# Performance work log

Measured on AMD Instinct MI355X. Metric: run time of the kernel, lower is better.

## Reference

```python
import jax, jax.numpy as jnp
import numpy as np
import math

B, N, D, H = 2, 2048, 512, 8
DH = D // H
HID = int(D * 16 / 3)  # 2730, SwiGLU hidden; chunks into 1365+1365
EPS = 1e-5


def _get_slopes(n):
    # n=8 is a power of two
    start = 2.0 ** (-2.0 ** (-(math.log2(n) - 3)))
    return np.array([start * (start ** i) for i in range(n)], dtype=np.float32)

_SLOPES = jnp.asarray(_get_slopes(H))  # [H]


def _ln(x, w, b):
    m = jnp.mean(x, axis=-1, keepdims=True)
    v = jnp.mean((x - m) ** 2, axis=-1, keepdims=True)
    return (x - m) * jax.lax.rsqrt(v + EPS) * w + b


def setup_inputs() -> dict:
    key = jax.random.key(0)
    ks = jax.random.split(key, 20)
    p = lambda k, s: jax.random.normal(k, s, jnp.float32) * 0.02
    return {
        "x": jax.random.normal(ks[0], (B, N, D), jnp.float32),
        "coords": jax.random.uniform(ks[1], (B, N, 2), jnp.float32) * 100.0,
        "q_w": p(ks[2], (D, D)), "q_b": jnp.zeros((D,), jnp.float32),
        "k_w": p(ks[3], (D, D)), "k_b": jnp.zeros((D,), jnp.float32),
        "v_w": p(ks[4], (D, D)), "v_b": jnp.zeros((D,), jnp.float32),
        "o_w": p(ks[5], (D, D)), "o_b": jnp.zeros((D,), jnp.float32),
        "gamma1": jnp.ones((D,), jnp.float32),
        "ln1_w": jnp.ones((D,), jnp.float32), "ln1_b": jnp.zeros((D,), jnp.float32),
        "fc1_w": p(ks[6], (HID, D)), "fc1_b": jnp.zeros((HID,), jnp.float32),
        "fc2_w": p(ks[7], (D, HID // 2)), "fc2_b": jnp.zeros((D,), jnp.float32),
        "gamma2": jnp.ones((D,), jnp.float32),
        "ln2_w": jnp.ones((D,), jnp.float32), "ln2_b": jnp.zeros((D,), jnp.float32),
    }


def reference(x, coords, q_w, q_b, k_w, k_b, v_w, v_b, o_w, o_b, gamma1,
              ln1_w, ln1_b, fc1_w, fc1_b, fc2_w, fc2_b, gamma2, ln2_w, ln2_b):
    # ---- residual1: distance-ALiBi attention (eval mode: x + gamma1*attn(norm(x)))
    xn = _ln(x, ln1_w, ln1_b)
    q = (xn @ q_w.T + q_b).reshape(B, N, H, DH).transpose(0, 2, 1, 3)  # [b,h,n,dh]
    k = (xn @ k_w.T + k_b).reshape(B, N, H, DH).transpose(0, 2, 1, 3)
    v = (xn @ v_w.T + v_b).reshape(B, N, H, DH).transpose(0, 2, 1, 3)
    # pairwise Euclidean distance of tile coords -> [b,n,n]
    diff = coords[:, :, None, :] - coords[:, None, :, :]
    dist = jnp.sqrt(jnp.sum(diff * diff, axis=-1))
    attn_bias = -_SLOPES[None, :, None, None] * dist[:, None, :, :]  # [b,h,n,n]
    scale = 1.0 / math.sqrt(DH)
    scores = jnp.einsum('bhqd,bhkd->bhqk', q, k) * scale + attn_bias
    attn = jax.nn.softmax(scores, axis=-1)
    ctx = jnp.einsum('bhqk,bhkd->bhqd', attn, v)
    ctx = ctx.transpose(0, 2, 1, 3).reshape(B, N, D)
    attn_out = ctx @ o_w.T + o_b
    x = x + gamma1 * attn_out
    # ---- residual2: SwiGLU-style MLP (eval mode: x + gamma2*mlp(norm(x)))
    xn2 = _ln(x, ln2_w, ln2_b)
    hpre = xn2 @ fc1_w.T + fc1_b  # [b,n,HID]
    h1, h2 = jnp.split(hpre, 2, axis=-1)
    mlp_out = (jax.nn.silu(h1) * h2) @ fc2_w.T + fc2_b
    return x + gamma2 * mlp_out
```

## Files before the change

kernel.cpp:

```cpp
#include <hip/hip_runtime.h>
#include <math.h>

#define Bdim  2
#define Nseq  2048
#define Dmod  512
#define Hn    8
#define DHd   64
#define HID   2730
#define HHALF 1365
#define HC    1408
#define NPACK 2816
#define ROWS  4096
#define NSPLIT 2
#define KT_PER (Nseq / 64 / NSPLIT)

typedef __bf16 bf16x8 __attribute__((ext_vector_type(8)));
typedef __bf16 bf16x4 __attribute__((ext_vector_type(4)));
typedef float  f32x4  __attribute__((ext_vector_type(4)));

__device__ __forceinline__ void glds16(const __bf16* g, __bf16* l) {
    __builtin_amdgcn_global_load_lds(
        (const __attribute__((address_space(1))) void*)g,
        (__attribute__((address_space(3))) void*)l, 16, 0, 0);
}

#define SEG0 (1536*512)
#define SEG1 (512*512)
#define SEG2 (NPACK*512)
#define SEG3 (512*HC)
__global__ __launch_bounds__(256) void convert_all(
    const float* __restrict__ q_w, const float* __restrict__ k_w,
    const float* __restrict__ v_w, const float* __restrict__ o_w,
    const float* __restrict__ fc1_w, const float* __restrict__ fc2_w,
    __bf16* __restrict__ wqkv, __bf16* __restrict__ wo,
    __bf16* __restrict__ wfc1p, __bf16* __restrict__ wfc2p)
{
    int idx = blockIdx.x * 256 + threadIdx.x;
    if (idx < SEG0) {
        int n = idx >> 9, k = idx & 511;
        float v = (n < 512) ? q_w[n * 512 + k]
                : (n < 1024) ? k_w[(n - 512) * 512 + k]
                : v_w[(n - 1024) * 512 + k];
        wqkv[idx] = (__bf16)v;
        return;
    }
    idx -= SEG0;
    if (idx < SEG1) { wo[idx] = (__bf16)o_w[idx]; return; }
    idx -= SEG1;
    if (idx < SEG2) {
        int n = idx >> 9, k = idx & 511;
        int j = n >> 5, u = n & 31;
        int base = j * 16 + (u & 15);
        float v = 0.0f;
        if (base < HHALF) {
            int hidx = base + ((u & 16) ? HHALF : 0);
            v = fc1_w[(size_t)hidx * 512 + k];
        }
        wfc1p[idx] = (__bf16)v;
        return;
    }
    idx -= SEG2;
    if (idx < SEG3) {
        int n = idx / HC, k = idx - n * HC;
        float v = (k < HHALF) ? fc2_w[(size_t)n * HHALF + k] : 0.0f;
        wfc2p[idx] = (__bf16)v;
    }
}

__global__ __launch_bounds__(256) void ln_kernel(
    const float* __restrict__ x, const float* __restrict__ w,
    const float* __restrict__ b, __bf16* __restrict__ out)
{
    const int row = blockIdx.x;
    const int tid = threadIdx.x;
    const float* xr = x + (size_t)row * Dmod;
    float2 v = *(const float2*)(xr + tid * 2);
    float s  = v.x + v.y;
    float sq = v.x * v.x + v.y * v.y;
#pragma unroll
    for (int m = 1; m < 64; m <<= 1) {
        s  += __shfl_xor(s, m, 64);
        sq += __shfl_xor(sq, m, 64);
    }
    __shared__ float ss[4], ssq[4];
    const int wv = tid >> 6;
    if ((tid & 63) == 0) { ss[wv] = s; ssq[wv] = sq; }
    __syncthreads();
    s  = ss[0] + ss[1] + ss[2] + ss[3];
    sq = ssq[0] + ssq[1] + ssq[2] + ssq[3];
    const float mean = s * (1.0f / Dmod);
    const float var  = sq * (1.0f / Dmod) - mean * mean;
    const float rstd = rsqrtf(var + 1e-5f);
    float2 wv2 = *(const float2*)(w + tid * 2);
    float2 bv2 = *(const float2*)(b + tid * 2);
    __bf16* orow = out + (size_t)row * Dmod + tid * 2;
    orow[0] = (__bf16)((v.x - mean) * rstd * wv2.x + bv2.x);
    orow[1] = (__bf16)((v.y - mean) * rstd * wv2.y + bv2.y);
}

__global__ __launch_bounds__(256) void gemm_res(
    const __bf16* __restrict__ A, int lda,
    const __bf16* __restrict__ Bw, int ldb,
    const float* __restrict__ bias, int K,
    float* __restrict__ out_f32, int ld_out,
    const float* __restrict__ res, const float* __restrict__ g)
{
    __shared__ __bf16 As[64][40];
    __shared__ __bf16 Bs[64][40];
    const int tid  = threadIdx.x;
    const int wave = tid >> 6, lane = tid & 63;
    const int t    = lane & 15, quad = lane >> 4;
    const int m0   = blockIdx.x * 64;
    const int n0   = blockIdx.y * 64;
    const int sr   = tid >> 2, sc = (tid & 3) * 8;

    f32x4 acc[4] = {};
    bf16x8 av = *(const bf16x8*)(A  + (size_t)(m0 + sr) * lda + sc);
    bf16x8 bv = *(const bf16x8*)(Bw + (size_t)(n0 + sr) * ldb + sc);

    for (int k0 = 0; k0 < K; k0 += 32) {
        __syncthreads();
        *(bf16x8*)(&As[sr][sc]) = av;
        *(bf16x8*)(&Bs[sr][sc]) = bv;
        __syncthreads();
        if (k0 + 32 < K) {
            av = *(const bf16x8*)(A  + (size_t)(m0 + sr) * lda + (k0 + 32 + sc));
            bv = *(const bf16x8*)(Bw + (size_t)(n0 + sr) * ldb + (k0 + 32 + sc));
        }
        bf16x8 a = *(const bf16x8*)(&As[wave * 16 + t][quad * 8]);
#pragma unroll
        for (int ct = 0; ct < 4; ++ct) {
            bf16x8 b = *(const bf16x8*)(&Bs[ct * 16 + t][quad * 8]);
            acc[ct] = __builtin_amdgcn_mfma_f32_16x16x32_bf16(a, b, acc[ct], 0, 0, 0);
        }
    }

    const int row_base = m0 + wave * 16 + quad * 4;
#pragma unroll
    for (int ct = 0; ct < 4; ++ct) {
        const int col = n0 + ct * 16 + t;
        const float bb = bias[col];
#pragma unroll
        for (int r = 0; r < 4; ++r) {
            const int row = row_base + r;
            out_f32[(size_t)row * ld_out + col] =
                res[(size_t)row * ld_out + col] + g[col] * (acc[ct][r] + bb);
        }
    }
}

__global__ __launch_bounds__(256) void qkv_gemm128(
    const __bf16* __restrict__ A, const __bf16* __restrict__ W,
    const float* __restrict__ qb_, const float* __restrict__ kb_,
    const float* __restrict__ vb_,
    __bf16* __restrict__ qk, __bf16* __restrict__ vtg)
{
    __shared__ __bf16 As[128 * 32];
    __shared__ __bf16 Bs[128 * 32];
    const int tid  = threadIdx.x;
    const int wave = tid >> 6, lane = tid & 63;
    const int t    = lane & 15, quad = lane >> 4;
    const int m0   = blockIdx.x * 128, n0 = blockIdx.y * 128;
    const int mr   = (wave & 1) * 64,  nr = (wave >> 1) * 64;
    const int ra0 = tid >> 2,          ca0 = (tid & 3) * 8;
    const int ra1 = (tid + 256) >> 2,  ca1 = (tid & 3) * 8;

    f32x4 acc[4][4] = {};

    for (int k0 = 0; k0 < Dmod; k0 += 32) {
        __syncthreads();
        glds16(A + (size_t)(m0 + ra0) * Dmod + k0 + ca0, As + tid * 8);
        glds16(A + (size_t)(m0 + ra1) * Dmod + k0 + ca1, As + (tid + 256) * 8);
        glds16(W + (size_t)(n0 + ra0) * Dmod + k0 + ca0, Bs + tid * 8);
        glds16(W + (size_t)(n0 + ra1) * Dmod + k0 + ca1, Bs + (tid + 256) * 8);
        __syncthreads();
        bf16x8 af[4], bfr[4];
#pragma unroll
        for (int mi = 0; mi < 4; ++mi)
            af[mi] = *(const bf16x8*)(As + (mr + mi * 16 + t) * 32 + quad * 8);
#pragma unroll
        for (int ni = 0; ni < 4; ++ni)
            bfr[ni] = *(const bf16x8*)(Bs + (nr + ni * 16 + t) * 32 + quad * 8);
#pragma unroll
        for (int mi = 0; mi < 4; ++mi)
#pragma unroll
            for (int ni = 0; ni < 4; ++ni)
                acc[mi][ni] = __builtin_amdgcn_mfma_f32_16x16x32_bf16(af[mi], bfr[ni], acc[mi][ni], 0, 0, 0);
    }

#pragma unroll
    for (int mi = 0; mi < 4; ++mi) {
        const int row_base = m0 + mr + mi * 16 + quad * 4;
#pragma unroll
        for (int ni = 0; ni < 4; ++ni) {
            const int col = n0 + nr + ni * 16 + t;
            const float bb = (col < 512) ? qb_[col]
                            : (col < 1024) ? kb_[col - 512] : vb_[col - 1024];
            if (col < 1024) {
#pragma unroll
                for (int r = 0; r < 4; ++r)
                    qk[(size_t)(row_base + r) * 1024 + col] = (__bf16)(acc[mi][ni][r] + bb);
            } else {
                const int f = col - 1024, hh = f >> 6, dh = f & 63;
                const int bI = row_base >> 11, n = row_base & 2047;
                bf16x4 pk;
#pragma unroll
                for (int r = 0; r < 4; ++r) pk[r] = (__bf16)(acc[mi][ni][r] + bb);
                *(bf16x4*)(vtg + ((size_t)((bI * 8 + hh) * 64 + dh)) * Nseq + n) = pk;
            }
        }
    }
}

__global__ __launch_bounds__(256) void fc1_gemm128(
    const __bf16* __restrict__ A, const __bf16* __restrict__ W,
    const float* __restrict__ fc1_b_, __bf16* __restrict__ out)
{
    __shared__ __bf16 As[128 * 32];
    __shared__ __bf16 Bs[128 * 32];
    const int tid  = threadIdx.x;
    const int wave = tid >> 6, lane = tid & 63;
    const int t    = lane & 15, quad = lane >> 4;
    const int m0   = blockIdx.x * 128, n0 = blockIdx.y * 128;
    const int mr   = (wave & 1) * 64,  nr = (wave >> 1) * 64;
    const int ra0 = tid >> 2,          ca0 = (tid & 3) * 8;
    const int ra1 = (tid + 256) >> 2,  ca1 = (tid & 3) * 8;

    f32x4 acc[4][4] = {};

    for (int k0 = 0; k0 < Dmod; k0 += 32) {
        __syncthreads();
        glds16(A + (size_t)(m0 + ra0) * Dmod + k0 + ca0, As + tid * 8);
        glds16(A + (size_t)(m0 + ra1) * Dmod + k0 + ca1, As + (tid + 256) * 8);
        glds16(W + (size_t)(n0 + ra0) * Dmod + k0 + ca0, Bs + tid * 8);
        glds16(W + (size_t)(n0 + ra1) * Dmod + k0 + ca1, Bs + (tid + 256) * 8);
        __syncthreads();
        bf16x8 af[4], bfr[4];
#pragma unroll
        for (int mi = 0; mi < 4; ++mi)
            af[mi] = *(const bf16x8*)(As + (mr + mi * 16 + t) * 32 + quad * 8);
#pragma unroll
        for (int ni = 0; ni < 4; ++ni)
            bfr[ni] = *(const bf16x8*)(Bs + (nr + ni * 16 + t) * 32 + quad * 8);
#pragma unroll
        for (int mi = 0; mi < 4; ++mi)
#pragma unroll
            for (int ni = 0; ni < 4; ++ni)
                acc[mi][ni] = __builtin_amdgcn_mfma_f32_16x16x32_bf16(af[mi], bfr[ni], acc[mi][ni], 0, 0, 0);
    }

#pragma unroll
    for (int mi = 0; mi < 4; ++mi) {
        const int row_base = m0 + mr + mi * 16 + quad * 4;
#pragma unroll
        for (int gI = 0; gI < 2; ++gI) {
            const int base = n0 + nr + gI * 32;
            const int hb = (base >> 5) * 16 + t;
            const bool valid = hb < HHALF;
            const float b1 = valid ? fc1_b_[hb] : 0.0f;
            const float b2 = valid ? fc1_b_[HHALF + hb] : 0.0f;
#pragma unroll
            for (int r = 0; r < 4; ++r) {
                float a = acc[mi][2 * gI][r] + b1;
                float c = acc[mi][2 * gI + 1][r] + b2;
                float sw = a / (1.0f + __expf(-a)) * c;
                out[(size_t)(row_base + r) * HC + hb] = (__bf16)sw;
            }
        }
    }
}

__global__ __launch_bounds__(256) void attn_kernel(
    const __bf16* __restrict__ qk, const __bf16* __restrict__ vt,
    const float* __restrict__ coords,
    float* __restrict__ op, float* __restrict__ lp)
{
    constexpr int LD = 72;
    __shared__ __bf16 Ks[64][LD];
    __shared__ __bf16 Vt[64][LD];
    __shared__ __bf16 Ps[64][LD];
    __shared__ float2 kco[64];

    const int qt = blockIdx.x, h = blockIdx.y;
    const int s = blockIdx.z >> 1, b = blockIdx.z & 1;
    const int bh = b * Hn + h;
    const int tid = threadIdx.x;
    const int wave = tid >> 6, lane = tid & 63;
    const int t = lane & 15, quad = lane >> 4;
    const float c1 = 0.125f * 1.44269504f;
    const float d1 = exp2f(-(float)(h + 1)) * 1.44269504f;
    const int kt0 = s * KT_PER, kt1 = kt0 + KT_PER;

    const int qrow = qt * 64 + wave * 16 + t;
    const size_t qbase = (size_t)(b * Nseq + qrow) * 1024 + h * DHd;
    bf16x8 bq0 = *(const bf16x8*)(qk + qbase + quad * 8);
    bf16x8 bq1 = *(const bf16x8*)(qk + qbase + 32 + quad * 8);
    float2 qc = *(const float2*)(coords + (size_t)(b * Nseq + qrow) * 2);
    const float qx = qc.x, qy = qc.y;

    const int sr = tid >> 3, scc = (tid & 7) * 8;
    const __bf16* kbase = qk + (size_t)(b * Nseq) * 1024 + 512 + h * DHd;
    const __bf16* vbase = vt + (size_t)(bh * 64) * Nseq;

    bf16x8 kreg0, kreg1, vreg0, vreg1;
    float2 kcreg = {0.f, 0.f};
    {
        const int kn0 = kt0 * 64;
        kreg0 = *(const bf16x8*)(kbase + (size_t)(kn0 + sr) * 1024 + scc);
        kreg1 = *(const bf16x8*)(kbase + (size_t)(kn0 + sr + 32) * 1024 + scc);
        vreg0 = *(const bf16x8*)(vbase + (size_t)sr * Nseq + kn0 + scc);
        vreg1 = *(const bf16x8*)(vbase + (size_t)(sr + 32) * Nseq + kn0 + scc);
        if (tid < 64) kcreg = *(const float2*)(coords + (size_t)(b * Nseq + kn0 + tid) * 2);
    }

    f32x4 o[4] = {};
    float lrun = 0.0f;

    for (int kt = kt0; kt < kt1; ++kt) {
        __syncthreads();
        *(bf16x8*)(&Ks[sr][scc])      = kreg0;
        *(bf16x8*)(&Ks[sr + 32][scc]) = kreg1;
        *(bf16x8*)(&Vt[sr][scc])      = vreg0;
        *(bf16x8*)(&Vt[sr + 32][scc]) = vreg1;
        if (tid < 64) kco[tid] = kcreg;
        __syncthreads();
        if (kt + 1 < kt1) {
            const int kn = (kt + 1) * 64;
            kreg0 = *(const bf16x8*)(kbase + (size_t)(kn + sr) * 1024 + scc);
            kreg1 = *(const bf16x8*)(kbase + (size_t)(kn + sr + 32) * 1024 + scc);
            vreg0 = *(const bf16x8*)(vbase + (size_t)sr * Nseq + kn + scc);
            vreg1 = *(const bf16x8*)(vbase + (size_t)(sr + 32) * Nseq + kn + scc);
            if (tid < 64) kcreg = *(const float2*)(coords + (size_t)(b * Nseq + kn + tid) * 2);
        }

        f32x4 sA[4];
#pragma unroll
        for (int am = 0; am < 4; ++am) {
            bf16x8 a0 = *(const bf16x8*)(&Ks[am * 16 + t][quad * 8]);
            bf16x8 a1 = *(const bf16x8*)(&Ks[am * 16 + t][32 + quad * 8]);
            f32x4 z = {};
            z = __builtin_amdgcn_mfma_f32_16x16x32_bf16(a0, bq0, z, 0, 0, 0);
            sA[am] = __builtin_amdgcn_mfma_f32_16x16x32_bf16(a1, bq1, z, 0, 0, 0);
        }

        float p[4][4];
#pragma unroll
        for (int am = 0; am < 4; ++am)
#pragma unroll
            for (int r = 0; r < 4; ++r) {
                float2 kc = kco[am * 16 + quad * 4 + r];
                float dx = qx - kc.x, dy = qy - kc.y;
                float dist = __builtin_amdgcn_sqrtf(dx * dx + dy * dy);
                float e = __builtin_amdgcn_exp2f(sA[am][r] * c1 - d1 * dist);
                p[am][r] = e;
                lrun += e;
            }

#pragma unroll
        for (int am = 0; am < 4; ++am) {
            bf16x4 pk;
#pragma unroll
            for (int r = 0; r < 4; ++r) pk[r] = (__bf16)p[am][r];
            *(bf16x4*)(&Ps[wave * 16 + t][am * 16 + quad * 4]) = pk;
        }

        bf16x8 ap0 = *(const bf16x8*)(&Ps[wave * 16 + t][quad * 8]);
        bf16x8 ap1 = *(const bf16x8*)(&Ps[wave * 16 + t][32 + quad * 8]);
#pragma unroll
        for (int ct = 0; ct < 4; ++ct) {
            bf16x8 bv0 = *(const bf16x8*)(&Vt[ct * 16 + t][quad * 8]);
            bf16x8 bv1 = *(const bf16x8*)(&Vt[ct * 16 + t][32 + quad * 8]);
            o[ct] = __builtin_amdgcn_mfma_f32_16x16x32_bf16(ap0, bv0, o[ct], 0, 0, 0);
            o[ct] = __builtin_amdgcn_mfma_f32_16x16x32_bf16(ap1, bv1, o[ct], 0, 0, 0);
        }
    }

    lrun += __shfl_xor(lrun, 16, 64);
    lrun += __shfl_xor(lrun, 32, 64);
    if (quad == 0)
        lp[(((size_t)s * Bdim + b) * Hn + h) * Nseq + qt * 64 + wave * 16 + t] = lrun;

    const int orow_base = qt * 64 + wave * 16 + quad * 4;
#pragma unroll
    for (int ct = 0; ct < 4; ++ct)
#pragma unroll
        for (int r = 0; r < 4; ++r) {
            size_t row = (size_t)s * ROWS + b * Nseq + orow_base + r;
            op[row * Dmod + h * DHd + ct * 16 + t] = o[ct][r];
        }
}

__global__ __launch_bounds__(256) void merge_kernel(
    const float* __restrict__ op, const float* __restrict__ lp,
    __bf16* __restrict__ ctx)
{
    int idx = blockIdx.x * 256 + threadIdx.x;
    int row = idx >> 7, c4 = (idx & 127) * 4;
    int h = c4 >> 6;
    int b = row >> 11, n = row & 2047;
    float l = lp[(((size_t)0 * Bdim + b) * Hn + h) * Nseq + n]
            + lp[(((size_t)1 * Bdim + b) * Hn + h) * Nseq + n];
    float rl = __builtin_amdgcn_rcpf(l);
    float4 o0 = *(const float4*)(op + (size_t)row * Dmod + c4);
    float4 o1 = *(const float4*)(op + ((size_t)ROWS + row) * Dmod + c4);
    bf16x4 r;
    r[0] = (__bf16)((o0.x + o1.x) * rl);
    r[1] = (__bf16)((o0.y + o1.y) * rl);
    r[2] = (__bf16)((o0.z + o1.z) * rl);
    r[3] = (__bf16)((o0.w + o1.w) * rl);
    *(bf16x4*)(ctx + (size_t)row * Dmod + c4) = r;
}

extern "C" void kernel_launch(void* const* d_in, const int* in_sizes, int n_in,
                              void* d_out, int out_size, void* d_ws, size_t ws_size,
                              hipStream_t stream)
{
    (void)in_sizes; (void)n_in; (void)out_size; (void)ws_size;
    const float* x      = (const float*)d_in[0];
    const float* coords = (const float*)d_in[1];
    const float* q_w    = (const float*)d_in[2];
    const float* q_b    = (const float*)d_in[3];
    const float* k_w    = (const float*)d_in[4];
    const float* k_b    = (const float*)d_in[5];
    const float* v_w    = (const float*)d_in[6];
    const float* v_b    = (const float*)d_in[7];
    const float* o_w    = (const float*)d_in[8];
    const float* o_b    = (const float*)d_in[9];
    const float* gamma1 = (const float*)d_in[10];
    const float* ln1_w  = (const float*)d_in[11];
    const float* ln1_b  = (const float*)d_in[12];
    const float* fc1_w  = (const float*)d_in[13];
    const float* fc1_b  = (const float*)d_in[14];
    const float* fc2_w  = (const float*)d_in[15];
    const float* fc2_b  = (const float*)d_in[16];
    const float* gamma2 = (const float*)d_in[17];
    const float* ln2_w  = (const float*)d_in[18];
    const float* ln2_b  = (const float*)d_in[19];

    size_t off = 0;
    auto alloc = [&](size_t bytes) {
        void* p = (char*)d_ws + off;
        off += (bytes + 255) & ~(size_t)255;
        return p;
    };
    __bf16* wqkv  = (__bf16*)alloc((size_t)1536 * 512 * 2);
    __bf16* wo    = (__bf16*)alloc((size_t)512 * 512 * 2);
    __bf16* wfc1p = (__bf16*)alloc((size_t)NPACK * 512 * 2);
    __bf16* wfc2p = (__bf16*)alloc((size_t)512 * HC * 2);
    __bf16* xn    = (__bf16*)alloc((size_t)ROWS * Dmod * 2);
    __bf16* xn2   = (__bf16*)alloc((size_t)ROWS * Dmod * 2);
    __bf16* qkb   = (__bf16*)alloc((size_t)ROWS * 1024 * 2);
    __bf16* vtg   = (__bf16*)alloc((size_t)Bdim * Hn * DHd * Nseq * 2);
    __bf16* ctxb  = (__bf16*)alloc((size_t)ROWS * Dmod * 2);
    float*  x1    = (float*)alloc((size_t)ROWS * Dmod * 4);
    __bf16* hcomb = (__bf16*)alloc((size_t)ROWS * HC * 2);
    float*  opb   = (float*)alloc((size_t)NSPLIT * ROWS * Dmod * 4);
    float*  lpb   = (float*)alloc((size_t)NSPLIT * Bdim * Hn * Nseq * 4);

    const int conv_total = SEG0 + SEG1 + SEG2 + SEG3;
    convert_all<<<(conv_total + 255) / 256, 256, 0, stream>>>(
        q_w, k_w, v_w, o_w, fc1_w, fc2_w, wqkv, wo, wfc1p, wfc2p);

    ln_kernel<<<ROWS, 256, 0, stream>>>(x, ln1_w, ln1_b, xn);

    qkv_gemm128<<<dim3(ROWS / 128, 12), 256, 0, stream>>>(xn, wqkv, q_b, k_b, v_b, qkb, vtg);

    attn_kernel<<<dim3(Nseq / 64, Hn, Bdim * NSPLIT), 256, 0, stream>>>(
        qkb, vtg, coords, opb, lpb);
    merge_kernel<<<(ROWS * 128 + 255) / 256, 256, 0, stream>>>(opb, lpb, ctxb);

    gemm_res<<<dim3(ROWS / 64, Dmod / 64), 256, 0, stream>>>(
        ctxb, Dmod, wo, Dmod, o_b, Dmod, x1, Dmod, x, gamma1);

    ln_kernel<<<ROWS, 256, 0, stream>>>(x1, ln2_w, ln2_b, xn2);

    fc1_gemm128<<<dim3(ROWS / 128, NPACK / 128), 256, 0, stream>>>(xn2, wfc1p, fc1_b, hcomb);

    gemm_res<<<dim3(ROWS / 64, Dmod / 64), 256, 0, stream>>>(
        hcomb, HC, wfc2p, HC, fc2_b, HC, (float*)d_out, Dmod, x1, gamma2);
}
```

Measured before the change: 229.8 us.

## Split attention keys four ways, stage V transpose via LDS, use direct LDS loads

Raises the key-split factor of attention from two to four so more blocks run concurrently, and generalizes the merge kernel to sum the four partial outputs and denominators. The QKV GEMM now handles V tiles by transposing through shared memory and writing coalesced 16-byte rows into the V^T buffer, where it previously did scattered 8-byte stores. The residual GEMM replaces register-staged prefetch with global_load_lds direct copies. The extra split adds partial-output traffic in the merge and relies on the workspace being large enough for four partials.

```diff
diff --git a/kernel.cpp b/kernel.cpp
--- a/kernel.cpp
+++ b/kernel.cpp
@@ -11,7 +11,7 @@
 #define HC    1408
 #define NPACK 2816
 #define ROWS  4096
-#define NSPLIT 2
+#define NSPLIT 4
 #define KT_PER (Nseq / 64 / NSPLIT)
 
 typedef __bf16 bf16x8 __attribute__((ext_vector_type(8)));
@@ -105,8 +105,8 @@
     float* __restrict__ out_f32, int ld_out,
     const float* __restrict__ res, const float* __restrict__ g)
 {
-    __shared__ __bf16 As[64][40];
-    __shared__ __bf16 Bs[64][40];
+    __shared__ __bf16 As[64 * 32];
+    __shared__ __bf16 Bs[64 * 32];
     const int tid  = threadIdx.x;
     const int wave = tid >> 6, lane = tid & 63;
     const int t    = lane & 15, quad = lane >> 4;
@@ -115,22 +115,16 @@
     const int sr   = tid >> 2, sc = (tid & 3) * 8;
 
     f32x4 acc[4] = {};
-    bf16x8 av = *(const bf16x8*)(A  + (size_t)(m0 + sr) * lda + sc);
-    bf16x8 bv = *(const bf16x8*)(Bw + (size_t)(n0 + sr) * ldb + sc);
 
     for (int k0 = 0; k0 < K; k0 += 32) {
         __syncthreads();
-        *(bf16x8*)(&As[sr][sc]) = av;
-        *(bf16x8*)(&Bs[sr][sc]) = bv;
-        __syncthreads();
-        if (k0 + 32 < K) {
-            av = *(const bf16x8*)(A  + (size_t)(m0 + sr) * lda + (k0 + 32 + sc));
-            bv = *(const bf16x8*)(Bw + (size_t)(n0 + sr) * ldb + (k0 + 32 + sc));
-        }
-        bf16x8 a = *(const bf16x8*)(&As[wave * 16 + t][quad * 8]);
+        glds16(A  + (size_t)(m0 + sr) * lda + k0 + sc, As + tid * 8);
+        glds16(Bw + (size_t)(n0 + sr) * ldb + k0 + sc, Bs + tid * 8);
+        __syncthreads();
+        bf16x8 a = *(const bf16x8*)(As + (wave * 16 + t) * 32 + quad * 8);
 #pragma unroll
         for (int ct = 0; ct < 4; ++ct) {
-            bf16x8 b = *(const bf16x8*)(&Bs[ct * 16 + t][quad * 8]);
+            bf16x8 b = *(const bf16x8*)(Bs + (ct * 16 + t) * 32 + quad * 8);
             acc[ct] = __builtin_amdgcn_mfma_f32_16x16x32_bf16(a, b, acc[ct], 0, 0, 0);
         }
     }
@@ -149,11 +143,99 @@
     }
 }
 
+#define LDT 136
 __global__ __launch_bounds__(256) void qkv_gemm128(
     const __bf16* __restrict__ A, const __bf16* __restrict__ W,
     const float* __restrict__ qb_, const float* __restrict__ kb_,
     const float* __restrict__ vb_,
     __bf16* __restrict__ qk, __bf16* __restrict__ vtg)
+{
+    __shared__ __bf16 smem[64 * LDT];
+    __bf16* As = smem;
+    __bf16* Bs = smem + 4096;
+    const int tid  = threadIdx.x;
+    const int wave = tid >> 6, lane = tid & 63;
+    const int t    = lane & 15, quad = lane >> 4;
+    const int m0   = blockIdx.x * 128, n0 = blockIdx.y * 128;
+    const int mr   = (wave & 1) * 64,  nr = (wave >> 1) * 64;
+    const int ra0 = tid >> 2,          ca0 = (tid & 3) * 8;
+    const int ra1 = (tid + 256) >> 2,  ca1 = (tid & 3) * 8;
+
+    f32x4 acc[4][4] = {};
+
+    for (int k0 = 0; k0 < Dmod; k0 += 32) {
+        __syncthreads();
+        glds16(A + (size_t)(m0 + ra0) * Dmod + k0 + ca0, As + tid * 8);
+        glds16(A + (size_t)(m0 + ra1) * Dmod + k0 + ca1, As + (tid + 256) * 8);
+        glds16(W + (size_t)(n0 + ra0) * Dmod + k0 + ca0, Bs + tid * 8);
+        glds16(W + (size_t)(n0 + ra1) * Dmod + k0 + ca1, Bs + (tid + 256) * 8);
+        __syncthreads();
+        bf16x8 af[4], bfr[4];
+#pragma unroll
+        for (int mi = 0; mi < 4; ++mi)
+            af[mi] = *(const bf16x8*)(As + (mr + mi * 16 + t) * 32 + quad * 8);
+#pragma unroll
+        for (int ni = 0; ni < 4; ++ni)
+            bfr[ni] = *(const bf16x8*)(Bs + (nr + ni * 16 + t) * 32 + quad * 8);
+#pragma unroll
+        for (int mi = 0; mi < 4; ++mi)
+#pragma unroll
+            for (int ni = 0; ni < 4; ++ni)
+                acc[mi][ni] = __builtin_amdgcn_mfma_f32_16x16x32_bf16(af[mi], bfr[ni], acc[mi][ni], 0, 0, 0);
+    }
+
+    const int y = blockIdx.y;
+    if (y < 8) {
+#pragma unroll
+        for (int mi = 0; mi < 4; ++mi) {
+            const int row_base = m0 + mr + mi * 16 + quad * 4;
+#pragma unroll
+            for (int ni = 0; ni < 4; ++ni) {
+                const int col = n0 + nr + ni * 16 + t;
+                const float bb = (col < 512) ? qb_[col] : kb_[col - 512];
+#pragma unroll
+                for (int r = 0; r < 4; ++r)
+                    qk[(size_t)(row_base + r) * 1024 + col] = (__bf16)(acc[mi][ni][r] + bb);
+            }
+        }
+    } else {
+        const int tok0 = m0 & 2047;
+        const int bI   = m0 >> 11;
+#pragma unroll
+        for (int half = 0; half < 2; ++half) {
+            __syncthreads();
+            if ((wave >> 1) == half) {
+#pragma unroll
+                for (int ni = 0; ni < 4; ++ni) {
+                    const int dh = ni * 16 + t;
+                    const float bb = vb_[(y - 8) * 128 + half * 64 + dh];
+#pragma unroll
+                    for (int mi = 0; mi < 4; ++mi) {
+                        const int n = mr + mi * 16 + quad * 4;
+                        bf16x4 pk;
+#pragma unroll
+                        for (int r = 0; r < 4; ++r) pk[r] = (__bf16)(acc[mi][ni][r] + bb);
+                        *(bf16x4*)(smem + dh * LDT + n) = pk;
+                    }
+                }
+            }
+            __syncthreads();
+            const int hh = (y - 8) * 2 + half;
+            const size_t rowbase = (size_t)(bI * 8 + hh) * 64;
+#pragma unroll
+            for (int j = 0; j < 4; ++j) {
+                int chunk = tid + j * 256;
+                int dr = chunk >> 4, cc = (chunk & 15) * 8;
+                bf16x8 vv = *(const bf16x8*)(smem + dr * LDT + cc);
+                *(bf16x8*)(vtg + (rowbase + dr) * Nseq + tok0 + cc) = vv;
+            }
+        }
+    }
+}
+
+__global__ __launch_bounds__(256) void fc1_gemm128(
+    const __bf16* __restrict__ A, const __bf16* __restrict__ W,
+    const float* __restrict__ fc1_b_, __bf16* __restrict__ out)
 {
     __shared__ __bf16 As[128 * 32];
     __shared__ __bf16 Bs[128 * 32];
@@ -192,67 +274,6 @@
     for (int mi = 0; mi < 4; ++mi) {
         const int row_base = m0 + mr + mi * 16 + quad * 4;
 #pragma unroll
-        for (int ni = 0; ni < 4; ++ni) {
-            const int col = n0 + nr + ni * 16 + t;
-            const float bb = (col < 512) ? qb_[col]
-                            : (col < 1024) ? kb_[col - 512] : vb_[col - 1024];
-            if (col < 1024) {
-#pragma unroll
-                for (int r = 0; r < 4; ++r)
-                    qk[(size_t)(row_base + r) * 1024 + col] = (__bf16)(acc[mi][ni][r] + bb);
-            } else {
-                const int f = col - 1024, hh = f >> 6, dh = f & 63;
-                const int bI = row_base >> 11, n = row_base & 2047;
-                bf16x4 pk;
-#pragma unroll
-                for (int r = 0; r < 4; ++r) pk[r] = (__bf16)(acc[mi][ni][r] + bb);
-                *(bf16x4*)(vtg + ((size_t)((bI * 8 + hh) * 64 + dh)) * Nseq + n) = pk;
-            }
-        }
-    }
-}
-
-__global__ __launch_bounds__(256) void fc1_gemm128(
-    const __bf16* __restrict__ A, const __bf16* __restrict__ W,
-    const float* __restrict__ fc1_b_, __bf16* __restrict__ out)
-{
-    __shared__ __bf16 As[128 * 32];
-    __shared__ __bf16 Bs[128 * 32];
-    const int tid  = threadIdx.x;
-    const int wave = tid >> 6, lane = tid & 63;
-    const int t    = lane & 15, quad = lane >> 4;
-    const int m0   = blockIdx.x * 128, n0 = blockIdx.y * 128;
-    const int mr   = (wave & 1) * 64,  nr = (wave >> 1) * 64;
-    const int ra0 = tid >> 2,          ca0 = (tid & 3) * 8;
-    const int ra1 = (tid + 256) >> 2,  ca1 = (tid & 3) * 8;
-
-    f32x4 acc[4][4] = {};
-
-    for (int k0 = 0; k0 < Dmod; k0 += 32) {
-        __syncthreads();
-        glds16(A + (size_t)(m0 + ra0) * Dmod + k0 + ca0, As + tid * 8);
-        glds16(A + (size_t)(m0 + ra1) * Dmod + k0 + ca1, As + (tid + 256) * 8);
-        glds16(W + (size_t)(n0 + ra0) * Dmod + k0 + ca0, Bs + tid * 8);
-        glds16(W + (size_t)(n0 + ra1) * Dmod + k0 + ca1, Bs + (tid + 256) * 8);
-        __syncthreads();
-        bf16x8 af[4], bfr[4];
-#pragma unroll
-        for (int mi = 0; mi < 4; ++mi)
-            af[mi] = *(const bf16x8*)(As + (mr + mi * 16 + t) * 32 + quad * 8);
-#pragma unroll
-        for (int ni = 0; ni < 4; ++ni)
-            bfr[ni] = *(const bf16x8*)(Bs + (nr + ni * 16 + t) * 32 + quad * 8);
-#pragma unroll
-        for (int mi = 0; mi < 4; ++mi)
-#pragma unroll
-            for (int ni = 0; ni < 4; ++ni)
-                acc[mi][ni] = __builtin_amdgcn_mfma_f32_16x16x32_bf16(af[mi], bfr[ni], acc[mi][ni], 0, 0, 0);
-    }
-
-#pragma unroll
-    for (int mi = 0; mi < 4; ++mi) {
-        const int row_base = m0 + mr + mi * 16 + quad * 4;
-#pragma unroll
         for (int gI = 0; gI < 2; ++gI) {
             const int base = n0 + nr + gI * 32;
             const int hb = (base >> 5) * 16 + t;
@@ -398,16 +419,22 @@
     int row = idx >> 7, c4 = (idx & 127) * 4;
     int h = c4 >> 6;
     int b = row >> 11, n = row & 2047;
-    float l = lp[(((size_t)0 * Bdim + b) * Hn + h) * Nseq + n]
-            + lp[(((size_t)1 * Bdim + b) * Hn + h) * Nseq + n];
+    float l = 0.0f;
+#pragma unroll
+    for (int s = 0; s < NSPLIT; ++s)
+        l += lp[(((size_t)s * Bdim + b) * Hn + h) * Nseq + n];
     float rl = __builtin_amdgcn_rcpf(l);
-    float4 o0 = *(const float4*)(op + (size_t)row * Dmod + c4);
-    float4 o1 = *(const float4*)(op + ((size_t)ROWS + row) * Dmod + c4);
+    float4 oa = {0.f, 0.f, 0.f, 0.f};
+#pragma unroll
+    for (int s = 0; s < NSPLIT; ++s) {
+        float4 ov = *(const float4*)(op + ((size_t)s * ROWS + row) * Dmod + c4);
+        oa.x += ov.x; oa.y += ov.y; oa.z += ov.z; oa.w += ov.w;
+    }
     bf16x4 r;
-    r[0] = (__bf16)((o0.x + o1.x) * rl);
-    r[1] = (__bf16)((o0.y + o1.y) * rl);
-    r[2] = (__bf16)((o0.z + o1.z) * rl);
-    r[3] = (__bf16)((o0.w + o1.w) * rl);
+    r[0] = (__bf16)(oa.x * rl);
+    r[1] = (__bf16)(oa.y * rl);
+    r[2] = (__bf16)(oa.z * rl);
+    r[3] = (__bf16)(oa.w * rl);
     *(bf16x4*)(ctx + (size_t)row * Dmod + c4) = r;
 }
 
```

Measured after the change: 236.7 us. +3.0%, slower.
